# Kernel optimization log

Hardware: AMD Instinct MI355X
Metric: run time of the kernel (lower is better)

Reference implementation:

```python
import jax, jax.numpy as jnp
import numpy as np

NEG_BIG = 1e8  # mask value from the original code


def setup_inputs() -> dict:
    key = jax.random.key(0)
    k1, k2, k3, k4, k5 = jax.random.split(key, 5)
    B, L, H, D = 16, 128, 256, 256
    # xavier-uniform-ish scale for the weight matrices
    lim = float(np.sqrt(6.0 / (H + D)))
    return {
        "encoder_output": jax.random.normal(k1, (B, L, H), dtype=jnp.float32),
        "W_l": jax.random.uniform(k2, (H, D), jnp.float32, -lim, lim),
        "W_r": jax.random.uniform(k3, (H, D), jnp.float32, -lim, lim),
        "U": jax.random.uniform(k4, (D,), jnp.float32, 0.0, 1.0),
        "logit_bias": jax.random.uniform(k5, (1,), jnp.float32, 0.0, 1.0),
    }


def reference(encoder_output, W_l, W_r, U, logit_bias):
    B, L, H = encoder_output.shape
    # projections: (B, L, D)
    dot_l = jnp.einsum("blh,hd->bld", encoder_output, W_l)
    dot_r = jnp.einsum("blh,hd->bld", encoder_output, W_r)
    # pairwise additive attention: (B, L, L, D) -> (B, L, L)
    final_sum = jnp.tanh(dot_l[:, :, None, :] + dot_r[:, None, :, :])
    logits = jnp.einsum("bijd,d->bij", final_sum, U) + logit_bias[0]
    # per-step diagonal mask (one_hot(i) at step i) vectorized as eye
    mask = jnp.eye(L, dtype=logits.dtype)  # (L, L)
    mask_scores = logits - NEG_BIG * mask[None, :, :]  # (B, L, L)
    probs = jax.nn.sigmoid(mask_scores)
    # Bernoulli sample (fixed key for reproducibility)
    samples = jax.random.bernoulli(jax.random.key(1), probs).astype(logits.dtype)  # graphs (B,L,L)
    # Bernoulli entropy: p*softplus(-l) + (1-p)*softplus(l), numerically stable
    entropy = probs * jax.nn.softplus(-mask_scores) + (1.0 - probs) * jax.nn.softplus(mask_scores)
    graph_batch = jnp.mean(samples, axis=0)  # (L, L)
    # BCE-with-logits mean over all elements (targets = sampled graphs)
    log_softmax = jnp.mean(jax.nn.softplus(mask_scores) - mask_scores * samples)
    entropy_regularization = jnp.mean(jnp.mean(entropy, axis=2), axis=1)  # (B,)
    return (mask_scores, samples, entropy, graph_batch, log_softmax, entropy_regularization)
```

## Files before the change

### kernel.cpp

```cpp
#include <hip/hip_runtime.h>

#define Bn 16
#define Ln 128
#define Hn 256
#define Dn 256

#define OFF_MASK   0
#define OFF_SMP    262144
#define OFF_ENT    524288
#define OFF_GRAPH  786432
#define OFF_LSE    802816
#define OFF_EREG   802817

static __device__ __forceinline__ unsigned rotl32(unsigned x, int r) {
  return (x << r) | (x >> (32 - r));
}

static __device__ __forceinline__ unsigned threefry_bits(unsigned c_hi, unsigned c_lo) {
  const unsigned ks0 = 0u, ks1 = 1u;
  const unsigned ks2 = 0u ^ 1u ^ 0x1BD11BDAu;
  unsigned x0 = c_hi + ks0;
  unsigned x1 = c_lo + ks1;
  x0 += x1; x1 = rotl32(x1, 13); x1 ^= x0;
  x0 += x1; x1 = rotl32(x1, 15); x1 ^= x0;
  x0 += x1; x1 = rotl32(x1, 26); x1 ^= x0;
  x0 += x1; x1 = rotl32(x1, 6);  x1 ^= x0;
  x0 += ks1; x1 += ks2 + 1u;
  x0 += x1; x1 = rotl32(x1, 17); x1 ^= x0;
  x0 += x1; x1 = rotl32(x1, 29); x1 ^= x0;
  x0 += x1; x1 = rotl32(x1, 16); x1 ^= x0;
  x0 += x1; x1 = rotl32(x1, 24); x1 ^= x0;
  x0 += ks2; x1 += ks0 + 2u;
  x0 += x1; x1 = rotl32(x1, 13); x1 ^= x0;
  x0 += x1; x1 = rotl32(x1, 15); x1 ^= x0;
  x0 += x1; x1 = rotl32(x1, 26); x1 ^= x0;
  x0 += x1; x1 = rotl32(x1, 6);  x1 ^= x0;
  x0 += ks0; x1 += ks1 + 3u;
  x0 += x1; x1 = rotl32(x1, 17); x1 ^= x0;
  x0 += x1; x1 = rotl32(x1, 29); x1 ^= x0;
  x0 += x1; x1 = rotl32(x1, 16); x1 ^= x0;
  x0 += x1; x1 = rotl32(x1, 24); x1 ^= x0;
  x0 += ks1; x1 += ks2 + 4u;
  x0 += x1; x1 = rotl32(x1, 13); x1 ^= x0;
  x0 += x1; x1 = rotl32(x1, 15); x1 ^= x0;
  x0 += x1; x1 = rotl32(x1, 26); x1 ^= x0;
  x0 += x1; x1 = rotl32(x1, 6);  x1 ^= x0;
  x0 += ks2; x1 += ks0 + 5u;
  return x0 ^ x1;
}

static __device__ __forceinline__ float softplus_f(float x) {
  return fmaxf(x, 0.0f) + log1pf(__expf(-fabsf(x)));
}

static __device__ __forceinline__ float fast_tanh(float x) {
  float e = __expf(-2.0f * x);
  float r = __builtin_amdgcn_rcpf(1.0f + e);
  return fmaf(2.0f, r, -1.0f);
}

__global__ void proj_kernel(const float* __restrict__ enc,
                            const float* __restrict__ Wl,
                            const float* __restrict__ Wr,
                            float* __restrict__ dl,
                            float* __restrict__ dr,
                            float* __restrict__ out,
                            double* __restrict__ ws_acc) {
  int gid = blockIdx.x * blockDim.x + threadIdx.x;
  if (gid < Ln * Ln) out[OFF_GRAPH + gid] = 0.0f;
  if (gid < 17) ws_acc[gid] = 0.0;

  int r0 = blockIdx.x * 4;
  int d = threadIdx.x;
  __shared__ float encS[4][Hn];
  ((float4*)encS)[d] = ((const float4*)(enc + (size_t)r0 * Hn))[d];
  __syncthreads();

  float al[4] = {0.f, 0.f, 0.f, 0.f};
  float ar[4] = {0.f, 0.f, 0.f, 0.f};
  for (int h4 = 0; h4 < Hn / 4; ++h4) {
    float4 e[4];
#pragma unroll
    for (int r = 0; r < 4; ++r) e[r] = ((const float4*)encS[r])[h4];
#pragma unroll
    for (int q = 0; q < 4; ++q) {
      int h = h4 * 4 + q;
      float wl = Wl[h * Dn + d];
      float wr = Wr[h * Dn + d];
#pragma unroll
      for (int r = 0; r < 4; ++r) {
        float ev = (q == 0) ? e[r].x : (q == 1) ? e[r].y : (q == 2) ? e[r].z : e[r].w;
        al[r] = fmaf(ev, wl, al[r]);
        ar[r] = fmaf(ev, wr, ar[r]);
      }
    }
  }
#pragma unroll
  for (int r = 0; r < 4; ++r) {
    dl[(size_t)(r0 + r) * Dn + d] = al[r];
    dr[(size_t)(r0 + r) * Dn + d] = ar[r];
  }
}

__global__ void pair_kernel(const float* __restrict__ dl,
                            const float* __restrict__ dr,
                            const float* __restrict__ U,
                            const float* __restrict__ bias,
                            float* __restrict__ out,
                            double* __restrict__ ws_acc) {
  int blk = blockIdx.x;
  int b = blk >> 6;
  int i0 = ((blk >> 1) & 31) * 4;
  int j0 = (blk & 1) * 64;
  int t = threadIdx.x;
  int dp = t & 15;
  int jj = t >> 4;

  __shared__ float dlS[4][Dn];
  __shared__ float pS[4][4 * 256];
  __shared__ float redS[8];

  ((float4*)dlS)[t] = ((const float4*)(dl + (size_t)(b * Ln + i0) * Dn))[t];

  float Ur[16];
  {
    const float4* U4 = (const float4*)(U + dp * 16);
#pragma unroll
    for (int q = 0; q < 4; ++q) {
      float4 u = U4[q];
      Ur[4*q+0] = u.x; Ur[4*q+1] = u.y; Ur[4*q+2] = u.z; Ur[4*q+3] = u.w;
    }
  }
  __syncthreads();

  float dlr[4][16];
#pragma unroll
  for (int r = 0; r < 4; ++r) {
#pragma unroll
    for (int q = 0; q < 4; ++q) {
      float4 a = *(const float4*)&dlS[r][dp * 16 + q * 4];
      dlr[r][4*q+0] = a.x; dlr[r][4*q+1] = a.y; dlr[r][4*q+2] = a.z; dlr[r][4*q+3] = a.w;
    }
  }

  const float* drt = dr + (size_t)b * Ln * Dn + (size_t)(j0 + jj) * Dn + dp * 16;
#pragma unroll
  for (int tl = 0; tl < 4; ++tl) {
    const float4* drp = (const float4*)(drt + (size_t)tl * 16 * Dn);
    float a0 = 0.f, a1 = 0.f, a2 = 0.f, a3 = 0.f;
#pragma unroll
    for (int q = 0; q < 4; ++q) {
      float4 v = drp[q];
#pragma unroll
      for (int c = 0; c < 4; ++c) {
        float dv = (c == 0) ? v.x : (c == 1) ? v.y : (c == 2) ? v.z : v.w;
        float uv = Ur[4*q+c];
        a0 = fmaf(fast_tanh(dlr[0][4*q+c] + dv), uv, a0);
        a1 = fmaf(fast_tanh(dlr[1][4*q+c] + dv), uv, a1);
        a2 = fmaf(fast_tanh(dlr[2][4*q+c] + dv), uv, a2);
        a3 = fmaf(fast_tanh(dlr[3][4*q+c] + dv), uv, a3);
      }
    }
    int sa = tl * 256 + jj * 16 + dp;
    pS[0][sa] = a0; pS[1][sa] = a1; pS[2][sa] = a2; pS[3][sa] = a3;
  }
  __syncthreads();

  int row = t >> 6;
  int jl = t & 63;
  int j = j0 + jl;
  const float* ps = &pS[row][(jl >> 4) * 256 + (jl & 15) * 16];
  float tot = 0.0f;
#pragma unroll
  for (int k = 0; k < 16; ++k) tot += ps[k];
  int i = i0 + row;
  float l = tot + bias[0] - ((j == i) ? 1.0e8f : 0.0f);
  float e = __expf(-l);
  float p = __builtin_amdgcn_rcpf(1.0f + e);
  unsigned n = ((unsigned)(b * Ln + i) << 7) | (unsigned)j;
  unsigned bits = threefry_bits(0u, n);
  float u = __uint_as_float((bits >> 9) | 0x3f800000u) - 1.0f;
  float smp = (u < p) ? 1.0f : 0.0f;
  float sp_pos = softplus_f(l);
  float sp_neg = softplus_f(-l);
  float ent = p * sp_neg + (1.0f - p) * sp_pos;
  size_t idx = (size_t)(b * Ln + i) * Ln + j;
  out[OFF_MASK + idx] = l;
  out[OFF_SMP + idx] = smp;
  out[OFF_ENT + idx] = ent;
  atomicAdd(&out[OFF_GRAPH + i * Ln + j], smp * 0.0625f);
  float ent_v = ent;
  float lse_v = sp_pos - l * smp;

#pragma unroll
  for (int off = 32; off > 0; off >>= 1) {
    ent_v += __shfl_down(ent_v, off);
    lse_v += __shfl_down(lse_v, off);
  }
  if ((t & 63) == 0) {
    redS[(t >> 6) * 2 + 0] = ent_v;
    redS[(t >> 6) * 2 + 1] = lse_v;
  }
  __syncthreads();
  if (t == 0) {
    float es = redS[0] + redS[2] + redS[4] + redS[6];
    float ls = redS[1] + redS[3] + redS[5] + redS[7];
    atomicAdd(&ws_acc[b], (double)es);
    atomicAdd(&ws_acc[16], (double)ls);
  }
}

__global__ void finalize_kernel(const double* __restrict__ ws_acc, float* __restrict__ out) {
  int t = threadIdx.x;
  if (t == 0) out[OFF_LSE] = (float)(ws_acc[16] / (double)(Bn * Ln * Ln));
  if (t < Bn) out[OFF_EREG + t] = (float)(ws_acc[t] / (double)(Ln * Ln));
}

extern "C" void kernel_launch(void* const* d_in, const int* in_sizes, int n_in,
                              void* d_out, int out_size, void* d_ws, size_t ws_size,
                              hipStream_t stream) {
  const float* enc = (const float*)d_in[0];
  const float* Wl = (const float*)d_in[1];
  const float* Wr = (const float*)d_in[2];
  const float* U = (const float*)d_in[3];
  const float* bias = (const float*)d_in[4];
  float* out = (float*)d_out;

  float* dl = (float*)d_ws;
  float* dr = dl + (size_t)Bn * Ln * Dn;
  double* ws_acc = (double*)(dr + (size_t)Bn * Ln * Dn);

  proj_kernel<<<Bn * Ln / 4, 256, 0, stream>>>(enc, Wl, Wr, dl, dr, out, ws_acc);
  pair_kernel<<<Bn * Ln / 2, 256, 0, stream>>>(dl, dr, U, bias, out, ws_acc);
  finalize_kernel<<<1, 64, 0, stream>>>(ws_acc, out);
}
```

Measured before the change: 114.7 us.

## Halve pair tile width, pad shared partials, fold finalize into last block

The pair kernel now covers 32 columns per block instead of 64, which doubles the grid to 2048 blocks and halves the per-thread tanh loop, so more blocks are available to fill the GPU. The shared-memory partial-sum buffer is padded to a stride of 17 to avoid bank conflicts and is much smaller. The separate finalize launch is replaced by a last-block-done atomic counter that writes the final means. In exchange, only half the threads take part in the epilogue, and per-block overhead and atomics roughly double.

```diff
diff --git a/kernel.cpp b/kernel.cpp
--- a/kernel.cpp
+++ b/kernel.cpp
@@ -68,7 +68,7 @@
                             double* __restrict__ ws_acc) {
   int gid = blockIdx.x * blockDim.x + threadIdx.x;
   if (gid < Ln * Ln) out[OFF_GRAPH + gid] = 0.0f;
-  if (gid < 17) ws_acc[gid] = 0.0;
+  if (gid < 18) ws_acc[gid] = 0.0;
 
   int r0 = blockIdx.x * 4;
   int d = threadIdx.x;
@@ -109,16 +109,16 @@
                             float* __restrict__ out,
                             double* __restrict__ ws_acc) {
   int blk = blockIdx.x;
-  int b = blk >> 6;
-  int i0 = ((blk >> 1) & 31) * 4;
-  int j0 = (blk & 1) * 64;
+  int b = blk >> 7;
+  int i0 = ((blk >> 2) & 31) * 4;
+  int j0 = (blk & 3) * 32;
   int t = threadIdx.x;
   int dp = t & 15;
   int jj = t >> 4;
 
   __shared__ float dlS[4][Dn];
-  __shared__ float pS[4][4 * 256];
-  __shared__ float redS[8];
+  __shared__ float pS[4][32 * 17];
+  __shared__ float redS[4];
 
   ((float4*)dlS)[t] = ((const float4*)(dl + (size_t)(b * Ln + i0) * Dn))[t];
 
@@ -145,7 +145,7 @@
 
   const float* drt = dr + (size_t)b * Ln * Dn + (size_t)(j0 + jj) * Dn + dp * 16;
 #pragma unroll
-  for (int tl = 0; tl < 4; ++tl) {
+  for (int tl = 0; tl < 2; ++tl) {
     const float4* drp = (const float4*)(drt + (size_t)tl * 16 * Dn);
     float a0 = 0.f, a1 = 0.f, a2 = 0.f, a3 = 0.f;
 #pragma unroll
@@ -161,59 +161,67 @@
         a3 = fmaf(fast_tanh(dlr[3][4*q+c] + dv), uv, a3);
       }
     }
-    int sa = tl * 256 + jj * 16 + dp;
+    int sa = (tl * 16 + jj) * 17 + dp;
     pS[0][sa] = a0; pS[1][sa] = a1; pS[2][sa] = a2; pS[3][sa] = a3;
   }
   __syncthreads();
 
-  int row = t >> 6;
-  int jl = t & 63;
-  int j = j0 + jl;
-  const float* ps = &pS[row][(jl >> 4) * 256 + (jl & 15) * 16];
-  float tot = 0.0f;
-#pragma unroll
-  for (int k = 0; k < 16; ++k) tot += ps[k];
-  int i = i0 + row;
-  float l = tot + bias[0] - ((j == i) ? 1.0e8f : 0.0f);
-  float e = __expf(-l);
-  float p = __builtin_amdgcn_rcpf(1.0f + e);
-  unsigned n = ((unsigned)(b * Ln + i) << 7) | (unsigned)j;
-  unsigned bits = threefry_bits(0u, n);
-  float u = __uint_as_float((bits >> 9) | 0x3f800000u) - 1.0f;
-  float smp = (u < p) ? 1.0f : 0.0f;
-  float sp_pos = softplus_f(l);
-  float sp_neg = softplus_f(-l);
-  float ent = p * sp_neg + (1.0f - p) * sp_pos;
-  size_t idx = (size_t)(b * Ln + i) * Ln + j;
-  out[OFF_MASK + idx] = l;
-  out[OFF_SMP + idx] = smp;
-  out[OFF_ENT + idx] = ent;
-  atomicAdd(&out[OFF_GRAPH + i * Ln + j], smp * 0.0625f);
-  float ent_v = ent;
-  float lse_v = sp_pos - l * smp;
+  float ent_v = 0.0f, lse_v = 0.0f;
+  if (t < 128) {
+    int row = t >> 5;
+    int jl = t & 31;
+    int j = j0 + jl;
+    const float* ps = &pS[row][jl * 17];
+    float tot = 0.0f;
+#pragma unroll
+    for (int k = 0; k < 16; ++k) tot += ps[k];
+    int i = i0 + row;
+    float l = tot + bias[0] - ((j == i) ? 1.0e8f : 0.0f);
+    float e = __expf(-l);
+    float p = __builtin_amdgcn_rcpf(1.0f + e);
+    unsigned n = ((unsigned)(b * Ln + i) << 7) | (unsigned)j;
+    unsigned bits = threefry_bits(0u, n);
+    float u = __uint_as_float((bits >> 9) | 0x3f800000u) - 1.0f;
+    float smp = (u < p) ? 1.0f : 0.0f;
+    float sp_pos = softplus_f(l);
+    float sp_neg = softplus_f(-l);
+    float ent = p * sp_neg + (1.0f - p) * sp_pos;
+    size_t idx = (size_t)(b * Ln + i) * Ln + j;
+    out[OFF_MASK + idx] = l;
+    out[OFF_SMP + idx] = smp;
+    out[OFF_ENT + idx] = ent;
+    atomicAdd(&out[OFF_GRAPH + i * Ln + j], smp * 0.0625f);
+    ent_v = ent;
+    lse_v = sp_pos - l * smp;
+  }
 
 #pragma unroll
   for (int off = 32; off > 0; off >>= 1) {
     ent_v += __shfl_down(ent_v, off);
     lse_v += __shfl_down(lse_v, off);
   }
-  if ((t & 63) == 0) {
+  if (((t & 63) == 0) && t < 128) {
     redS[(t >> 6) * 2 + 0] = ent_v;
     redS[(t >> 6) * 2 + 1] = lse_v;
   }
   __syncthreads();
   if (t == 0) {
-    float es = redS[0] + redS[2] + redS[4] + redS[6];
-    float ls = redS[1] + redS[3] + redS[5] + redS[7];
+    float es = redS[0] + redS[2];
+    float ls = redS[1] + redS[3];
     atomicAdd(&ws_acc[b], (double)es);
     atomicAdd(&ws_acc[16], (double)ls);
-  }
-}
-
-__global__ void finalize_kernel(const double* __restrict__ ws_acc, float* __restrict__ out) {
-  int t = threadIdx.x;
-  if (t == 0) out[OFF_LSE] = (float)(ws_acc[16] / (double)(Bn * Ln * Ln));
-  if (t < Bn) out[OFF_EREG + t] = (float)(ws_acc[t] / (double)(Ln * Ln));
+    __threadfence();
+    unsigned int* ctr = (unsigned int*)&ws_acc[17];
+    unsigned done = atomicAdd(ctr, 1u);
+    if (done == (unsigned)(gridDim.x - 1)) {
+      double ls_tot = atomicAdd(&ws_acc[16], 0.0);
+      out[OFF_LSE] = (float)(ls_tot / (double)(Bn * Ln * Ln));
+      for (int q = 0; q < Bn; ++q) {
+        double ev = atomicAdd(&ws_acc[q], 0.0);
+        out[OFF_EREG + q] = (float)(ev / (double)(Ln * Ln));
+      }
+    }
+  }
 }
 
 extern "C" void kernel_launch(void* const* d_in, const int* in_sizes, int n_in,
@@ -231,6 +239,5 @@
   double* ws_acc = (double*)(dr + (size_t)Bn * Ln * Dn);
 
   proj_kernel<<<Bn * Ln / 4, 256, 0, stream>>>(enc, Wl, Wr, dl, dr, out, ws_acc);
-  pair_kernel<<<Bn * Ln / 2, 256, 0, stream>>>(dl, dr, U, bias, out, ws_acc);
-  finalize_kernel<<<1, 64, 0, stream>>>(ws_acc, out);
-}
+  pair_kernel<<<Bn * Ln, 256, 0, stream>>>(dl, dr, U, bias, out, ws_acc);
+}
```

Result: slower. 158.6 us (+38.3%).
